# Kernel optimization log

Measured on AMD Instinct MI355X. Metric: run time of the kernel, lower is better.

The kernel has to match this reference:

```python
import jax, jax.numpy as jnp
import numpy as np
from jax import lax

T, B, F = 4096, 32, 3
L = 4                 # num_ema_layers
D = 64                # num_features / d_model
DI = 2 * D            # mamba d_inner (expand=2)
DS = 16               # d_state
DTR = 4               # dt_rank = ceil(D/16)
KC = 4                # conv kernel size
EPS = 1e-6


def setup_inputs() -> dict:
    key = jax.random.key(0)
    ks = jax.random.split(key, 16)
    s = 0.02
    inp = {
        "x": jax.random.normal(ks[0], (T, B, F), jnp.float32),
        # in_proj: (F*L) -> D
        "W_in": jax.random.normal(ks[1], (F * L, D), jnp.float32) * s,
        "b_in": jnp.zeros((D,), jnp.float32),
        # pre-mamba RMSNorm scale
        "rms_scale": jnp.ones((D,), jnp.float32),
        # mamba in_proj: D -> 2*DI
        "mW_in": jax.random.normal(ks[2], (D, 2 * DI), jnp.float32) * s,
        "mb_in": jnp.zeros((2 * DI,), jnp.float32),
        # depthwise causal conv over time: [DI, KC]
        "convW": jax.random.normal(ks[3], (DI, KC), jnp.float32) * s,
        "convb": jnp.zeros((DI,), jnp.float32),
        # x_proj: DI -> dt_rank + 2*DS
        "W_xp": jax.random.normal(ks[4], (DI, DTR + 2 * DS), jnp.float32) * s,
        # dt_proj: dt_rank -> DI
        "W_dt": jax.random.normal(ks[5], (DTR, DI), jnp.float32) * s,
        "b_dt": jnp.full((DI,), -4.6, jnp.float32),  # softplus(-4.6) ~ 0.01 init dt
        # SSM params
        "A_log": jnp.log(jnp.broadcast_to(jnp.arange(1, DS + 1, dtype=jnp.float32), (DI, DS))),
        "Dp": jnp.ones((DI,), jnp.float32),
        # mamba out_proj: DI -> D
        "W_out": jax.random.normal(ks[6], (DI, D), jnp.float32) * s,
        "b_out": jnp.zeros((D,), jnp.float32),
        # sim_proj: D -> 3
        "W_sim": jax.random.normal(ks[7], (D, 3), jnp.float32) * s,
        "b_sim": jnp.zeros((3,), jnp.float32),
    }
    return inp


def _ema_std(x):
    # x: [T, B, F] -> standardized per EMA layer: [T, B, F, L]
    alphas = 2.0 ** -jnp.arange(1, L + 1, dtype=jnp.float32)  # [L]

    def step(carry, xt):
        m, v = carry                      # [B, F, L]
        xt = xt[..., None]                # [B, F, 1]
        m = alphas * xt + (1 - alphas) * m
        v = alphas * xt * xt + (1 - alphas) * v
        var = jnp.maximum(v - m * m, 0.0)
        out = (xt - m) / jnp.sqrt(var + EPS)
        return (m, v), out

    init = (jnp.zeros((B, F, L), jnp.float32), jnp.zeros((B, F, L), jnp.float32))
    _, ys = lax.scan(step, init, x)
    return ys  # [T, B, F, L]


def _rmsnorm(x, scale):
    var = jnp.mean(x * x, axis=-1, keepdims=True)
    return x * lax.rsqrt(var + EPS) * scale


def _mamba(x, mW_in, mb_in, convW, convb, W_xp, W_dt, b_dt, A_log, Dp, W_out, b_out):
    # x: [T, B, D]
    u = x @ mW_in + mb_in                  # [T, B, 2*DI]
    xm, res = u[..., :DI], u[..., DI:]
    # causal depthwise conv along time (kernel KC)
    xpad = jnp.concatenate([jnp.zeros((KC - 1, B, DI), x.dtype), xm], axis=0)
    xc = sum(convW[:, k] * xpad[k:k + T] for k in range(KC)) + convb
    xc = jax.nn.silu(xc)                   # [T, B, DI]

    xp = xc @ W_xp                         # [T, B, DTR + 2*DS]
    delta = jax.nn.softplus(xp[..., :DTR] @ W_dt + b_dt)   # [T, B, DI]
    Bm = xp[..., DTR:DTR + DS]             # [T, B, DS]
    Cm = xp[..., DTR + DS:]                # [T, B, DS]
    A = -jnp.exp(A_log)                    # [DI, DS]

    def sstep(h, inp):
        d_t, B_t, C_t, x_t = inp           # [B,DI],[B,DS],[B,DS],[B,DI]
        dA = jnp.exp(d_t[..., None] * A)   # [B, DI, DS]
        h = dA * h + (d_t * x_t)[..., None] * B_t[:, None, :]
        y = jnp.einsum('bds,bs->bd', h, C_t)
        return h, y

    h0 = jnp.zeros((B, DI, DS), x.dtype)
    _, ys = lax.scan(sstep, h0, (delta, Bm, Cm, xc))
    y = ys + Dp * xc                       # [T, B, DI]
    y = y * jax.nn.silu(res)
    return y @ W_out + b_out               # [T, B, D]


def reference(x, W_in, b_in, rms_scale, mW_in, mb_in, convW, convb,
              W_xp, W_dt, b_dt, A_log, Dp, W_out, b_out, W_sim, b_sim):
    xe = _ema_std(x)                               # [T, B, F, L]
    h = xe.reshape(T, B, F * L) @ W_in + b_in      # [T, B, D]
    hn = _rmsnorm(h, rms_scale)
    h = h + _mamba(hn, mW_in, mb_in, convW, convb, W_xp, W_dt, b_dt,
                   A_log, Dp, W_out, b_out)        # residual Mamba block
    return h @ W_sim + b_sim                       # [T, B, 3] logits
```

## Files before the change

kernel.cpp:

```cpp
#include <hip/hip_runtime.h>
#include <hip/hip_bf16.h>
#include <math.h>

#define T_    4096
#define B_    32
#define F_    3
#define L_    4
#define D_    64
#define DI_   128
#define DS_   16
#define DTR_  4
#define KC_   4
#define NXP_  36
#define EPS_  1e-6f

#define CH_   128
#define NC_   (T_/CH_)
#define CHE_  64
#define NCE_  (T_/CHE_)

#define XE_OFF    ((size_t)0)
#define H_OFF     (XE_OFF   + (size_t)T_*B_*12)
#define XM_OFF    (H_OFF    + (size_t)T_*B_*64)
#define SRES_OFF  (XM_OFF   + (size_t)T_*B_*128)
#define XP_OFF    (SRES_OFF + (size_t)T_*B_*128)
#define HEND_OFF  (XP_OFF   + (size_t)T_*B_*36)
#define SUMD_OFF  (HEND_OFF + (size_t)NC_*B_*DI_*DS_)
#define HST_OFF   (SUMD_OFF + (size_t)NC_*B_*DI_)
#define EME_OFF   (HST_OFF  + (size_t)NC_*B_*DI_*DS_)
#define EVE_OFF   (EME_OFF  + (size_t)NCE_*B_*F_*L_)
#define EMS_OFF   (EVE_OFF  + (size_t)NCE_*B_*F_*L_)
#define EVS_OFF   (EMS_OFF  + (size_t)NCE_*B_*F_*L_)
#define FOLD_OFF  (EVS_OFF  + (size_t)NCE_*B_*F_*L_)

__device__ __forceinline__ float sigmoidf_(float x) { return 1.f / (1.f + __expf(-x)); }
__device__ __forceinline__ float softplusf_(float x) {
    return fmaxf(x, 0.f) + log1pf(__expf(-fabsf(x)));
}

__global__ __launch_bounds__(256) void ema_phase1(const float* __restrict__ x,
                                                  float* __restrict__ me, float* __restrict__ ve) {
    int tid = blockIdx.x * blockDim.x + threadIdx.x;
    if (tid >= NCE_ * B_ * F_) return;
    int c = tid / (B_ * F_);
    int r = tid % (B_ * F_);
    int b = r / F_, f = r % F_;
    const float al[L_] = {0.5f, 0.25f, 0.125f, 0.0625f};
    float m[L_] = {0,0,0,0}, v[L_] = {0,0,0,0};
    int t0 = c * CHE_;
    for (int i = 0; i < CHE_; ++i) {
        float xv = x[((t0 + i) * B_ + b) * F_ + f];
        #pragma unroll
        for (int l = 0; l < L_; ++l) {
            m[l] = al[l] * xv      + (1.f - al[l]) * m[l];
            v[l] = al[l] * xv * xv + (1.f - al[l]) * v[l];
        }
    }
    int o = ((c * B_ + b) * F_ + f) * L_;
    #pragma unroll
    for (int l = 0; l < L_; ++l) { me[o + l] = m[l]; ve[o + l] = v[l]; }
}

__global__ __launch_bounds__(256) void ema_combine(const float* __restrict__ me, const float* __restrict__ ve,
                                                   float* __restrict__ ms, float* __restrict__ vs) {
    int tid = blockIdx.x * blockDim.x + threadIdx.x;
    if (tid >= B_ * F_ * L_) return;
    int l = tid % L_;
    int f = (tid / L_) % F_;
    int b = tid / (L_ * F_);
    const float al[L_] = {0.5f, 0.25f, 0.125f, 0.0625f};
    float dec = powf(1.f - al[l], (float)CHE_);
    float m = 0.f, v = 0.f;
    for (int c = 0; c < NCE_; ++c) {
        int o = ((c * B_ + b) * F_ + f) * L_ + l;
        ms[o] = m; vs[o] = v;
        m = dec * m + me[o];
        v = dec * v + ve[o];
    }
}

__global__ __launch_bounds__(256) void ema_phase3(const float* __restrict__ x,
                                                  const float* __restrict__ ms, const float* __restrict__ vs,
                                                  float* __restrict__ xe) {
    int tid = blockIdx.x * blockDim.x + threadIdx.x;
    if (tid >= NCE_ * B_ * F_) return;
    int c = tid / (B_ * F_);
    int r = tid % (B_ * F_);
    int b = r / F_, f = r % F_;
    const float al[L_] = {0.5f, 0.25f, 0.125f, 0.0625f};
    float m[L_], v[L_];
    int o = ((c * B_ + b) * F_ + f) * L_;
    #pragma unroll
    for (int l = 0; l < L_; ++l) { m[l] = ms[o + l]; v[l] = vs[o + l]; }
    int t0 = c * CHE_;
    for (int i = 0; i < CHE_; ++i) {
        int t = t0 + i;
        float xv = x[(t * B_ + b) * F_ + f];
        float4 ov;
        float* op = (float*)&ov;
        #pragma unroll
        for (int l = 0; l < L_; ++l) {
            m[l] = al[l] * xv      + (1.f - al[l]) * m[l];
            v[l] = al[l] * xv * xv + (1.f - al[l]) * v[l];
            float var = fmaxf(v[l] - m[l] * m[l], 0.f);
            op[l] = (xv - m[l]) * rsqrtf(var + EPS_);
        }
        *(float4*)&xe[((size_t)t * B_ + b) * 12 + f * 4] = ov;
    }
}

__global__ __launch_bounds__(256) void gemm_in(
    const float* __restrict__ xe_g, const float* __restrict__ W_in, const float* __restrict__ b_in,
    const float* __restrict__ rms_scale, const float* __restrict__ mW_in, const float* __restrict__ mb_in,
    float* __restrict__ h_g, float* __restrict__ xm_g, float* __restrict__ sres_g)
{
    __shared__ __align__(16) float s_xe[64 * 12];
    __shared__ __align__(16) float s_hn[64 * 64];
    __shared__ __align__(16) float s_Win[12 * 64];
    int tid = threadIdx.x;
    size_t g0 = (size_t)blockIdx.x * 64;

    for (int i = tid; i < 12 * 64; i += 256) s_Win[i] = W_in[i];
    for (int i = tid; i < 64 * 12; i += 256) s_xe[i] = xe_g[g0 * 12 + i];
    __syncthreads();

    int lane = tid & 63, w = tid >> 6;
    float bin = b_in[lane], scl = rms_scale[lane];
    #pragma unroll 4
    for (int i = 0; i < 16; ++i) {
        int r = w * 16 + i;
        float hv = bin;
        #pragma unroll
        for (int k = 0; k < 12; ++k) hv += s_xe[r * 12 + k] * s_Win[k * 64 + lane];
        h_g[(g0 + r) * 64 + lane] = hv;
        float ss = hv * hv;
        #pragma unroll
        for (int off = 32; off; off >>= 1) ss += __shfl_xor(ss, off);
        s_hn[r * 64 + lane] = hv * rsqrtf(ss * (1.f / 64.f) + EPS_) * scl;
    }

    float wc[64];
    #pragma unroll
    for (int k = 0; k < 64; ++k) wc[k] = mW_in[k * 256 + tid];
    float mb = mb_in[tid];
    __syncthreads();

    bool isres = tid >= 128;
    float* outp = isres ? (sres_g + g0 * 128 + (tid - 128)) : (xm_g + g0 * 128 + tid);
    for (int r = 0; r < 64; ++r) {
        float u = mb;
        const float4* hn4 = (const float4*)(s_hn + r * 64);
        #pragma unroll
        for (int q = 0; q < 16; ++q) {
            float4 hh = hn4[q];
            u += hh.x * wc[4*q] + hh.y * wc[4*q+1] + hh.z * wc[4*q+2] + hh.w * wc[4*q+3];
        }
        if (isres) u = u * sigmoidf_(u);
        outp[(size_t)r * 128] = u;
    }
}

#define XCPAD 132
__global__ __launch_bounds__(256) void conv_xp(
    const float* __restrict__ xm_g, const float* __restrict__ convW, const float* __restrict__ convb,
    const float* __restrict__ W_xp, float* __restrict__ xp_g)
{
    int t = blockIdx.x;
    int tid = threadIdx.x;
    __shared__ __align__(16) float s_xc[32 * XCPAD];
    __shared__ __align__(16) float s_Wxp[128 * 36];
    __shared__ __align__(16) float s_convWT[4 * 128];
    __shared__ __align__(16) float s_convb[128];

    for (int i = tid; i < 128 * 36; i += 256) s_Wxp[i] = W_xp[i];
    for (int i = tid; i < 512; i += 256) s_convWT[(i & 3) * 128 + (i >> 2)] = convW[i];
    if (tid < 128) s_convb[tid] = convb[tid];
    __syncthreads();

    #pragma unroll
    for (int i = tid; i < 4096; i += 256) {
        int b = i >> 7, j = i & 127;
        float acc = s_convb[j];
        #pragma unroll
        for (int k = 0; k < 4; ++k) {
            int tt = t - 3 + k;
            float xv = (tt >= 0) ? xm_g[((size_t)tt * 32 + b) * 128 + j] : 0.f;
            acc += s_convWT[k * 128 + j] * xv;
        }
        acc = acc * sigmoidf_(acc);
        s_xc[b * XCPAD + j] = acc;
    }
    __syncthreads();

    int b = tid >> 3, q = tid & 7;
    float acc[36];
    #pragma unroll
    for (int o = 0; o < 36; ++o) acc[o] = 0.f;
    #pragma unroll
    for (int dd = 0; dd < 16; ++dd) {
        int d = q + dd * 8;
        float xv = s_xc[b * XCPAD + d];
        const float* wr = s_Wxp + d * 36;
        #pragma unroll
        for (int o = 0; o < 36; ++o) acc[o] += xv * wr[o];
    }
    #pragma unroll
    for (int o = 0; o < 36; ++o) {
        acc[o] += __shfl_xor(acc[o], 1);
        acc[o] += __shfl_xor(acc[o], 2);
        acc[o] += __shfl_xor(acc[o], 4);
    }
    if (q == 0) {
        float* xpo = xp_g + ((size_t)t * 32 + b) * 36;
        #pragma unroll
        for (int o4 = 0; o4 < 9; ++o4)
            *(float4*)&xpo[o4 * 4] = make_float4(acc[o4*4], acc[o4*4+1], acc[o4*4+2], acc[o4*4+3]);
    }
}

__global__ __launch_bounds__(128) void ssm_phase1(
    const float* __restrict__ xm_g, const float* __restrict__ xp_g,
    const float* __restrict__ convW, const float* __restrict__ convb,
    const float* __restrict__ W_dt, const float* __restrict__ b_dt, const float* __restrict__ A_log,
    float* __restrict__ hend_g, float* __restrict__ sumd_g)
{
    int c = blockIdx.x >> 5;
    int b = blockIdx.x & 31;
    int j = threadIdx.x;
    float Ar[16], hs[16];
    #pragma unroll
    for (int s = 0; s < 16; ++s) { Ar[s] = -__expf(A_log[j * 16 + s]); hs[s] = 0.f; }
    float wdt[4];
    #pragma unroll
    for (int i = 0; i < 4; ++i) wdt[i] = W_dt[i * 128 + j];
    float bdt = b_dt[j];
    float cw0 = convW[j*4+0], cw1 = convW[j*4+1], cw2 = convW[j*4+2], cw3 = convW[j*4+3];
    float cb = convb[j];
    int t0 = c * CH_;
    float x3 = 0.f, x2 = 0.f, x1 = 0.f;
    if (t0 >= 3) {
        x3 = xm_g[((size_t)(t0-3) * 32 + b) * 128 + j];
        x2 = xm_g[((size_t)(t0-2) * 32 + b) * 128 + j];
        x1 = xm_g[((size_t)(t0-1) * 32 + b) * 128 + j];
    }
    float sumd = 0.f;
    for (int it = 0; it < CH_; ++it) {
        size_t row = (size_t)(t0 + it) * 32 + b;
        float x0 = xm_g[row * 128 + j];
        float xc = cb + cw0 * x3 + cw1 * x2 + cw2 * x1 + cw3 * x0;
        x3 = x2; x2 = x1; x1 = x0;
        xc = xc * sigmoidf_(xc);
        const float4* xp4 = (const float4*)(xp_g + row * 36);
        float4 dt4 = xp4[0];
        float z = bdt + dt4.x * wdt[0] + dt4.y * wdt[1] + dt4.z * wdt[2] + dt4.w * wdt[3];
        float dl = softplusf_(z);
        sumd += dl;
        float dx = dl * xc;
        #pragma unroll
        for (int qq = 0; qq < 4; ++qq) {
            float4 Bm = xp4[1 + qq];
            float* bp = (float*)&Bm;
            #pragma unroll
            for (int u = 0; u < 4; ++u) {
                int s = qq * 4 + u;
                hs[s] = __expf(dl * Ar[s]) * hs[s] + dx * bp[u];
            }
        }
    }
    size_t cbk = (size_t)blockIdx.x;
    #pragma unroll
    for (int s = 0; s < 16; ++s) hend_g[(cbk * 16 + s) * 128 + j] = hs[s];
    sumd_g[cbk * 128 + j] = sumd;
}

__global__ __launch_bounds__(256) void ssm_combine(
    const float* __restrict__ A_log, const float* __restrict__ hend,
    const float* __restrict__ sumd, float* __restrict__ hstart)
{
    int tid = blockIdx.x * 256 + threadIdx.x;
    int d = tid & 127;
    int s = (tid >> 7) & 15;
    int b = tid >> 11;
    float A = -__expf(A_log[d * 16 + s]);
    float h = 0.f;
    for (int c = 0; c < NC_; ++c) {
        size_t cb = (size_t)(c * 32 + b);
        hstart[(cb * 16 + s) * 128 + d] = h;
        h = __expf(A * sumd[cb * 128 + d]) * h + hend[(cb * 16 + s) * 128 + d];
    }
}

__global__ __launch_bounds__(128) void ssm_phase3(
    const float* __restrict__ xm_g, const float* __restrict__ xp_g, float* sres_y,
    const float* __restrict__ hstart, const float* __restrict__ convW, const float* __restrict__ convb,
    const float* __restrict__ W_dt, const float* __restrict__ b_dt, const float* __restrict__ A_log,
    const float* __restrict__ Dp)
{
    int c = blockIdx.x >> 5;
    int b = blockIdx.x & 31;
    int j = threadIdx.x;
    size_t cbk = (size_t)blockIdx.x;
    float Ar[16], hs[16];
    #pragma unroll
    for (int s = 0; s < 16; ++s) {
        Ar[s] = -__expf(A_log[j * 16 + s]);
        hs[s] = hstart[(cbk * 16 + s) * 128 + j];
    }
    float wdt[4];
    #pragma unroll
    for (int i = 0; i < 4; ++i) wdt[i] = W_dt[i * 128 + j];
    float bdt = b_dt[j];
    float cw0 = convW[j*4+0], cw1 = convW[j*4+1], cw2 = convW[j*4+2], cw3 = convW[j*4+3];
    float cb = convb[j];
    float dp = Dp[j];
    int t0 = c * CH_;
    float x3 = 0.f, x2 = 0.f, x1 = 0.f;
    if (t0 >= 3) {
        x3 = xm_g[((size_t)(t0-3) * 32 + b) * 128 + j];
        x2 = xm_g[((size_t)(t0-2) * 32 + b) * 128 + j];
        x1 = xm_g[((size_t)(t0-1) * 32 + b) * 128 + j];
    }
    for (int it = 0; it < CH_; ++it) {
        size_t row = (size_t)(t0 + it) * 32 + b;
        float x0 = xm_g[row * 128 + j];
        float xc = cb + cw0 * x3 + cw1 * x2 + cw2 * x1 + cw3 * x0;
        x3 = x2; x2 = x1; x1 = x0;
        xc = xc * sigmoidf_(xc);
        const float4* xp4 = (const float4*)(xp_g + row * 36);
        float4 dt4 = xp4[0];
        float z = bdt + dt4.x * wdt[0] + dt4.y * wdt[1] + dt4.z * wdt[2] + dt4.w * wdt[3];
        float dl = softplusf_(z);
        float dx = dl * xc;
        float y = 0.f;
        #pragma unroll
        for (int qq = 0; qq < 4; ++qq) {
            float4 Bm = xp4[1 + qq];
            float4 Cm = xp4[5 + qq];
            float* bp = (float*)&Bm;
            float* cp = (float*)&Cm;
            #pragma unroll
            for (int u = 0; u < 4; ++u) {
                int s = qq * 4 + u;
                hs[s] = __expf(dl * Ar[s]) * hs[s] + dx * bp[u];
                y += hs[s] * cp[u];
            }
        }
        float sr = sres_y[row * 128 + j];
        sres_y[row * 128 + j] = (y + dp * xc) * sr;
    }
}

__global__ __launch_bounds__(256) void fold_w(
    const float* __restrict__ W_out, const float* __restrict__ b_out,
    const float* __restrict__ W_sim, const float* __restrict__ b_sim, float* __restrict__ fold)
{
    int tid = threadIdx.x;
    for (int i = tid; i < 384; i += 256) {
        int d = i / 3, o = i % 3;
        float a = 0.f;
        for (int k = 0; k < 64; ++k) a += W_out[d * 64 + k] * W_sim[k * 3 + o];
        fold[i] = a;
    }
    if (tid < 3) {
        float a = b_sim[tid];
        for (int k = 0; k < 64; ++k) a += b_out[k] * W_sim[k * 3 + tid];
        fold[384 + tid] = a;
    }
}

__global__ __launch_bounds__(256) void out_gemm(
    const float* __restrict__ y_g, const float* __restrict__ h_g,
    const float* __restrict__ W_sim, const float* __restrict__ fold, float* __restrict__ out)
{
    __shared__ __align__(16) float s_Wc[384];
    __shared__ __align__(16) float s_Ws[192];
    __shared__ float s_bsc[3];
    int tid = threadIdx.x;
    for (int i = tid; i < 384; i += 256) s_Wc[i] = fold[i];
    for (int i = tid; i < 192; i += 256) s_Ws[i] = W_sim[i];
    if (tid < 3) s_bsc[tid] = fold[384 + tid];
    __syncthreads();

    int lane = tid & 63, wid = tid >> 6;
    size_t row0 = (size_t)blockIdx.x * 128;
    for (int it = 0; it < 32; ++it) {
        size_t row = row0 + it * 4 + wid;
        const float* yr = y_g + row * 128;
        float y1 = yr[lane], y2 = yr[64 + lane];
        float hv = h_g[row * 64 + lane];
        float p0 = y1 * s_Wc[lane*3+0] + y2 * s_Wc[(64+lane)*3+0] + hv * s_Ws[lane*3+0];
        float p1 = y1 * s_Wc[lane*3+1] + y2 * s_Wc[(64+lane)*3+1] + hv * s_Ws[lane*3+1];
        float p2 = y1 * s_Wc[lane*3+2] + y2 * s_Wc[(64+lane)*3+2] + hv * s_Ws[lane*3+2];
        #pragma unroll
        for (int off = 32; off; off >>= 1) {
            p0 += __shfl_xor(p0, off);
            p1 += __shfl_xor(p1, off);
            p2 += __shfl_xor(p2, off);
        }
        if (lane == 0) {
            out[row * 3 + 0] = p0 + s_bsc[0];
            out[row * 3 + 1] = p1 + s_bsc[1];
            out[row * 3 + 2] = p2 + s_bsc[2];
        }
    }
}

extern "C" void kernel_launch(void* const* d_in, const int* in_sizes, int n_in,
                              void* d_out, int out_size, void* d_ws, size_t ws_size,
                              hipStream_t stream) {
    const float* x         = (const float*)d_in[0];
    const float* W_in      = (const float*)d_in[1];
    const float* b_in      = (const float*)d_in[2];
    const float* rms_scale = (const float*)d_in[3];
    const float* mW_in     = (const float*)d_in[4];
    const float* mb_in     = (const float*)d_in[5];
    const float* convW     = (const float*)d_in[6];
    const float* convb     = (const float*)d_in[7];
    const float* W_xp      = (const float*)d_in[8];
    const float* W_dt      = (const float*)d_in[9];
    const float* b_dt      = (const float*)d_in[10];
    const float* A_log     = (const float*)d_in[11];
    const float* Dp        = (const float*)d_in[12];
    const float* W_out     = (const float*)d_in[13];
    const float* b_out     = (const float*)d_in[14];
    const float* W_sim     = (const float*)d_in[15];
    const float* b_sim     = (const float*)d_in[16];
    float* out = (float*)d_out;
    float* ws  = (float*)d_ws;

    float* xe    = ws + XE_OFF;
    float* h_g   = ws + H_OFF;
    float* xm_g  = ws + XM_OFF;
    float* sres  = ws + SRES_OFF;
    float* xp_g  = ws + XP_OFF;
    float* hend  = ws + HEND_OFF;
    float* sumd  = ws + SUMD_OFF;
    float* hstart= ws + HST_OFF;
    float* eme   = ws + EME_OFF;
    float* eve   = ws + EVE_OFF;
    float* ems   = ws + EMS_OFF;
    float* evs   = ws + EVS_OFF;
    float* fold  = ws + FOLD_OFF;

    ema_phase1<<<(NCE_*B_*F_ + 255)/256, 256, 0, stream>>>(x, eme, eve);
    ema_combine<<<(B_*F_*L_ + 255)/256, 256, 0, stream>>>(eme, eve, ems, evs);
    ema_phase3<<<(NCE_*B_*F_ + 255)/256, 256, 0, stream>>>(x, ems, evs, xe);
    fold_w<<<1, 256, 0, stream>>>(W_out, b_out, W_sim, b_sim, fold);
    gemm_in<<<T_*B_/64, 256, 0, stream>>>(xe, W_in, b_in, rms_scale, mW_in, mb_in,
                                          h_g, xm_g, sres);
    conv_xp<<<T_, 256, 0, stream>>>(xm_g, convW, convb, W_xp, xp_g);
    ssm_phase1<<<NC_*B_, 128, 0, stream>>>(xm_g, xp_g, convW, convb, W_dt, b_dt, A_log,
                                           hend, sumd);
    ssm_combine<<<(B_*DI_*DS_)/256, 256, 0, stream>>>(A_log, hend, sumd, hstart);
    ssm_phase3<<<NC_*B_, 128, 0, stream>>>(xm_g, xp_g, sres, hstart, convW, convb,
                                           W_dt, b_dt, A_log, Dp);
    out_gemm<<<T_*B_/128, 256, 0, stream>>>(sres, h_g, W_sim, fold, out);
}
```

Before: 681.0 us.

## Split SSM state across thread pairs, halve chunk size, prefetch inputs, in-place combine

The chunked SSM scan now gives each channel two threads, each owning 8 of the 16 state entries, and sums the output contributions with a lane shuffle. The chunk length drops from 128 to 64, so there are more blocks and a shorter serial loop per thread. Each iteration also prefetches the next timestep's inputs. The chunk-end state layout becomes [chunk,b,d,s] so it can be stored with float4, and the combine pass writes the chunk-start states back into the same buffer instead of a separate one. The trade-off is that the sequential combine loop gets twice as many chunks and the dt/conv/softplus work is done redundantly by both threads of a pair.

```diff
diff --git a/kernel.cpp b/kernel.cpp
--- a/kernel.cpp
+++ b/kernel.cpp
@@ -14,7 +14,7 @@
 #define NXP_  36
 #define EPS_  1e-6f
 
-#define CH_   128
+#define CH_   64
 #define NC_   (T_/CH_)
 #define CHE_  64
 #define NCE_  (T_/CHE_)
@@ -26,8 +26,7 @@
 #define XP_OFF    (SRES_OFF + (size_t)T_*B_*128)
 #define HEND_OFF  (XP_OFF   + (size_t)T_*B_*36)
 #define SUMD_OFF  (HEND_OFF + (size_t)NC_*B_*DI_*DS_)
-#define HST_OFF   (SUMD_OFF + (size_t)NC_*B_*DI_)
-#define EME_OFF   (HST_OFF  + (size_t)NC_*B_*DI_*DS_)
+#define EME_OFF   (SUMD_OFF + (size_t)NC_*B_*DI_)
 #define EVE_OFF   (EME_OFF  + (size_t)NCE_*B_*F_*L_)
 #define EMS_OFF   (EVE_OFF  + (size_t)NCE_*B_*F_*L_)
 #define EVS_OFF   (EMS_OFF  + (size_t)NCE_*B_*F_*L_)
@@ -218,7 +217,7 @@
     }
 }
 
-__global__ __launch_bounds__(128) void ssm_phase1(
+__global__ __launch_bounds__(256) void ssm_phase1(
     const float* __restrict__ xm_g, const float* __restrict__ xp_g,
     const float* __restrict__ convW, const float* __restrict__ convb,
     const float* __restrict__ W_dt, const float* __restrict__ b_dt, const float* __restrict__ A_log,
@@ -226,127 +225,154 @@
 {
     int c = blockIdx.x >> 5;
     int b = blockIdx.x & 31;
-    int j = threadIdx.x;
-    float Ar[16], hs[16];
-    #pragma unroll
-    for (int s = 0; s < 16; ++s) { Ar[s] = -__expf(A_log[j * 16 + s]); hs[s] = 0.f; }
-    float wdt[4];
-    #pragma unroll
-    for (int i = 0; i < 4; ++i) wdt[i] = W_dt[i * 128 + j];
+    int tid = threadIdx.x;
+    int j = tid >> 1, sh = tid & 1;
+    float Ar[8], hs[8];
+    #pragma unroll
+    for (int u = 0; u < 8; ++u) { Ar[u] = -__expf(A_log[j * 16 + sh * 8 + u]); hs[u] = 0.f; }
+    float wdt0 = W_dt[j], wdt1 = W_dt[128 + j], wdt2 = W_dt[256 + j], wdt3 = W_dt[384 + j];
     float bdt = b_dt[j];
     float cw0 = convW[j*4+0], cw1 = convW[j*4+1], cw2 = convW[j*4+2], cw3 = convW[j*4+3];
-    float cb = convb[j];
+    float cbv = convb[j];
     int t0 = c * CH_;
     float x3 = 0.f, x2 = 0.f, x1 = 0.f;
-    if (t0 >= 3) {
+    if (c > 0) {
         x3 = xm_g[((size_t)(t0-3) * 32 + b) * 128 + j];
         x2 = xm_g[((size_t)(t0-2) * 32 + b) * 128 + j];
         x1 = xm_g[((size_t)(t0-1) * 32 + b) * 128 + j];
     }
     float sumd = 0.f;
+    float nx; float4 nd, nB0, nB1;
+    {
+        size_t row = (size_t)t0 * 32 + b;
+        nx = xm_g[row * 128 + j];
+        const float4* xp4 = (const float4*)(xp_g + row * 36);
+        nd = xp4[0]; nB0 = xp4[1 + 2*sh]; nB1 = xp4[2 + 2*sh];
+    }
     for (int it = 0; it < CH_; ++it) {
-        size_t row = (size_t)(t0 + it) * 32 + b;
-        float x0 = xm_g[row * 128 + j];
-        float xc = cb + cw0 * x3 + cw1 * x2 + cw2 * x1 + cw3 * x0;
+        float x0 = nx; float4 dt4 = nd, B0 = nB0, B1 = nB1;
+        {
+            int tn = t0 + it + 1; if (tn > T_ - 1) tn = T_ - 1;
+            size_t row = (size_t)tn * 32 + b;
+            nx = xm_g[row * 128 + j];
+            const float4* xp4 = (const float4*)(xp_g + row * 36);
+            nd = xp4[0]; nB0 = xp4[1 + 2*sh]; nB1 = xp4[2 + 2*sh];
+        }
+        float xc = cbv + cw0*x3 + cw1*x2 + cw2*x1 + cw3*x0;
         x3 = x2; x2 = x1; x1 = x0;
         xc = xc * sigmoidf_(xc);
-        const float4* xp4 = (const float4*)(xp_g + row * 36);
-        float4 dt4 = xp4[0];
-        float z = bdt + dt4.x * wdt[0] + dt4.y * wdt[1] + dt4.z * wdt[2] + dt4.w * wdt[3];
+        float z = bdt + dt4.x*wdt0 + dt4.y*wdt1 + dt4.z*wdt2 + dt4.w*wdt3;
         float dl = softplusf_(z);
         sumd += dl;
         float dx = dl * xc;
-        #pragma unroll
-        for (int qq = 0; qq < 4; ++qq) {
-            float4 Bm = xp4[1 + qq];
-            float* bp = (float*)&Bm;
-            #pragma unroll
-            for (int u = 0; u < 4; ++u) {
-                int s = qq * 4 + u;
-                hs[s] = __expf(dl * Ar[s]) * hs[s] + dx * bp[u];
-            }
-        }
+        const float* bp0 = (const float*)&B0;
+        const float* bp1 = (const float*)&B1;
+        #pragma unroll
+        for (int u = 0; u < 4; ++u) hs[u]     = __expf(dl * Ar[u])     * hs[u]     + dx * bp0[u];
+        #pragma unroll
+        for (int u = 0; u < 4; ++u) hs[4 + u] = __expf(dl * Ar[4 + u]) * hs[4 + u] + dx * bp1[u];
     }
     size_t cbk = (size_t)blockIdx.x;
-    #pragma unroll
-    for (int s = 0; s < 16; ++s) hend_g[(cbk * 16 + s) * 128 + j] = hs[s];
-    sumd_g[cbk * 128 + j] = sumd;
+    float4* he = (float4*)&hend_g[(cbk * 128 + j) * 16 + sh * 8];
+    he[0] = make_float4(hs[0], hs[1], hs[2], hs[3]);
+    he[1] = make_float4(hs[4], hs[5], hs[6], hs[7]);
+    if (sh == 0) sumd_g[cbk * 128 + j] = sumd;
 }
 
 __global__ __launch_bounds__(256) void ssm_combine(
-    const float* __restrict__ A_log, const float* __restrict__ hend,
-    const float* __restrict__ sumd, float* __restrict__ hstart)
+    const float* __restrict__ A_log, float* __restrict__ hend, const float* __restrict__ sumd)
 {
     int tid = blockIdx.x * 256 + threadIdx.x;
-    int d = tid & 127;
-    int s = (tid >> 7) & 15;
+    int s = tid & 15;
+    int d = (tid >> 4) & 127;
     int b = tid >> 11;
     float A = -__expf(A_log[d * 16 + s]);
     float h = 0.f;
     for (int c = 0; c < NC_; ++c) {
         size_t cb = (size_t)(c * 32 + b);
-        hstart[(cb * 16 + s) * 128 + d] = h;
-        h = __expf(A * sumd[cb * 128 + d]) * h + hend[(cb * 16 + s) * 128 + d];
-    }
-}
-
-__global__ __launch_bounds__(128) void ssm_phase3(
-    const float* __restrict__ xm_g, const float* __restrict__ xp_g, float* sres_y,
+        size_t o = (cb * 128 + d) * 16 + s;
+        float tmp = hend[o];
+        hend[o] = h;
+        h = __expf(A * sumd[cb * 128 + d]) * h + tmp;
+    }
+}
+
+__global__ __launch_bounds__(256) void ssm_phase3(
+    const float* __restrict__ xm_g, const float* __restrict__ xp_g, float* __restrict__ sres_y,
     const float* __restrict__ hstart, const float* __restrict__ convW, const float* __restrict__ convb,
     const float* __restrict__ W_dt, const float* __restrict__ b_dt, const float* __restrict__ A_log,
     const float* __restrict__ Dp)
 {
     int c = blockIdx.x >> 5;
     int b = blockIdx.x & 31;
-    int j = threadIdx.x;
+    int tid = threadIdx.x;
+    int j = tid >> 1, sh = tid & 1;
     size_t cbk = (size_t)blockIdx.x;
-    float Ar[16], hs[16];
-    #pragma unroll
-    for (int s = 0; s < 16; ++s) {
-        Ar[s] = -__expf(A_log[j * 16 + s]);
-        hs[s] = hstart[(cbk * 16 + s) * 128 + j];
-    }
-    float wdt[4];
-    #pragma unroll
-    for (int i = 0; i < 4; ++i) wdt[i] = W_dt[i * 128 + j];
+    float Ar[8], hs[8];
+    #pragma unroll
+    for (int u = 0; u < 8; ++u) Ar[u] = -__expf(A_log[j * 16 + sh * 8 + u]);
+    {
+        const float4* h4 = (const float4*)&hstart[(cbk * 128 + j) * 16 + sh * 8];
+        float4 a = h4[0], bb = h4[1];
+        hs[0]=a.x; hs[1]=a.y; hs[2]=a.z; hs[3]=a.w;
+        hs[4]=bb.x; hs[5]=bb.y; hs[6]=bb.z; hs[7]=bb.w;
+    }
+    float wdt0 = W_dt[j], wdt1 = W_dt[128 + j], wdt2 = W_dt[256 + j], wdt3 = W_dt[384 + j];
     float bdt = b_dt[j];
     float cw0 = convW[j*4+0], cw1 = convW[j*4+1], cw2 = convW[j*4+2], cw3 = convW[j*4+3];
-    float cb = convb[j];
+    float cbv = convb[j];
     float dp = Dp[j];
     int t0 = c * CH_;
     float x3 = 0.f, x2 = 0.f, x1 = 0.f;
-    if (t0 >= 3) {
+    if (c > 0) {
         x3 = xm_g[((size_t)(t0-3) * 32 + b) * 128 + j];
         x2 = xm_g[((size_t)(t0-2) * 32 + b) * 128 + j];
         x1 = xm_g[((size_t)(t0-1) * 32 + b) * 128 + j];
     }
+    float nx; float4 nd;
+    {
+        size_t row = (size_t)t0 * 32 + b;
+        nx = xm_g[row * 128 + j];
+        nd = *(const float4*)(xp_g + row * 36);
+    }
     for (int it = 0; it < CH_; ++it) {
+        float x0 = nx; float4 dt4 = nd;
         size_t row = (size_t)(t0 + it) * 32 + b;
-        float x0 = xm_g[row * 128 + j];
-        float xc = cb + cw0 * x3 + cw1 * x2 + cw2 * x1 + cw3 * x0;
+        const float4* xp4 = (const float4*)(xp_g + row * 36);
+        float4 B0 = xp4[1 + 2*sh], B1 = xp4[2 + 2*sh];
+        float4 C0 = xp4[5 + 2*sh], C1 = xp4[6 + 2*sh];
+        {
+            int tn = t0 + it + 1; if (tn > T_ - 1) tn = T_ - 1;
+            size_t rown = (size_t)tn * 32 + b;
+            nx = xm_g[rown * 128 + j];
+            nd = *(const float4*)(xp_g + rown * 36);
+        }
+        float xc = cbv + cw0*x3 + cw1*x2 + cw2*x1 + cw3*x0;
         x3 = x2; x2 = x1; x1 = x0;
         xc = xc * sigmoidf_(xc);
-        const float4* xp4 = (const float4*)(xp_g + row * 36);
-        float4 dt4 = xp4[0];
-        float z = bdt + dt4.x * wdt[0] + dt4.y * wdt[1] + dt4.z * wdt[2] + dt4.w * wdt[3];
+        float z = bdt + dt4.x*wdt0 + dt4.y*wdt1 + dt4.z*wdt2 + dt4.w*wdt3;
         float dl = softplusf_(z);
         float dx = dl * xc;
         float y = 0.f;
-        #pragma unroll
-        for (int qq = 0; qq < 4; ++qq) {
-            float4 Bm = xp4[1 + qq];
-            float4 Cm = xp4[5 + qq];
-            float* bp = (float*)&Bm;
-            float* cp = (float*)&Cm;
-            #pragma unroll
-            for (int u = 0; u < 4; ++u) {
-                int s = qq * 4 + u;
-                hs[s] = __expf(dl * Ar[s]) * hs[s] + dx * bp[u];
-                y += hs[s] * cp[u];
-            }
-        }
-        float sr = sres_y[row * 128 + j];
-        sres_y[row * 128 + j] = (y + dp * xc) * sr;
+        const float* bp0 = (const float*)&B0;
+        const float* bp1 = (const float*)&B1;
+        const float* cp0 = (const float*)&C0;
+        const float* cp1 = (const float*)&C1;
+        #pragma unroll
+        for (int u = 0; u < 4; ++u) {
+            hs[u] = __expf(dl * Ar[u]) * hs[u] + dx * bp0[u];
+            y += hs[u] * cp0[u];
+        }
+        #pragma unroll
+        for (int u = 0; u < 4; ++u) {
+            hs[4+u] = __expf(dl * Ar[4+u]) * hs[4+u] + dx * bp1[u];
+            y += hs[4+u] * cp1[u];
+        }
+        y += __shfl_xor(y, 1);
+        if (sh == 0) {
+            float sr = sres_y[row * 128 + j];
+            sres_y[row * 128 + j] = (y + dp * xc) * sr;
+        }
     }
 }
 
@@ -435,7 +461,6 @@
     float* xp_g  = ws + XP_OFF;
     float* hend  = ws + HEND_OFF;
     float* sumd  = ws + SUMD_OFF;
-    float* hstart= ws + HST_OFF;
     float* eme   = ws + EME_OFF;
     float* eve   = ws + EVE_OFF;
     float* ems   = ws + EMS_OFF;
@@ -449,10 +474,10 @@
     gemm_in<<<T_*B_/64, 256, 0, stream>>>(xe, W_in, b_in, rms_scale, mW_in, mb_in,
                                           h_g, xm_g, sres);
     conv_xp<<<T_, 256, 0, stream>>>(xm_g, convW, convb, W_xp, xp_g);
-    ssm_phase1<<<NC_*B_, 128, 0, stream>>>(xm_g, xp_g, convW, convb, W_dt, b_dt, A_log,
+    ssm_phase1<<<NC_*B_, 256, 0, stream>>>(xm_g, xp_g, convW, convb, W_dt, b_dt, A_log,
                                            hend, sumd);
-    ssm_combine<<<(B_*DI_*DS_)/256, 256, 0, stream>>>(A_log, hend, sumd, hstart);
-    ssm_phase3<<<NC_*B_, 128, 0, stream>>>(xm_g, xp_g, sres, hstart, convW, convb,
+    ssm_combine<<<(B_*DI_*DS_)/256, 256, 0, stream>>>(A_log, hend, sumd);
+    ssm_phase3<<<NC_*B_, 256, 0, stream>>>(xm_g, xp_g, sres, hend, convW, convb,
                                            W_dt, b_dt, A_log, Dp);
     out_gemm<<<T_*B_/128, 256, 0, stream>>>(sres, h_g, W_sim, fold, out);
 }
```

Result: slower. 722.9 us (+6.1%).
